# Optimization experiments

Hardware: AMD Instinct MI355X
Metric: run time of the kernel (lower is better)

## Reference

```python
import jax, jax.numpy as jnp
import numpy as np

HIDDEN_DIM = 2048
NUM_HEADS = 16
HEAD_DIM = HIDDEN_DIM // NUM_HEADS  # 128, used only as softmax temperature sqrt(HEAD_DIM)
RING_SIZE = 4
RANK = 0  # dist not initialized


def _hilbert_mapping(size: int) -> np.ndarray:
    """Boustrophedon (snake) scan over a ceil(sqrt(size)) grid; mapping[pos] = scan index."""
    grid = int(np.ceil(np.sqrt(size)))
    order = []
    for row in range(grid):
        cols = range(grid) if row % 2 == 0 else range(grid - 1, -1, -1)
        for col in cols:
            pos = row * grid + col
            if pos < size:
                order.append(pos)
    mapping = np.zeros(size, dtype=np.int64)
    mapping[np.asarray(order)] = np.arange(size, dtype=np.int64)
    return mapping


def setup_inputs() -> dict:
    key = jax.random.key(0)
    k1, k2 = jax.random.split(key)
    batch, seq_len = 2, 8192
    chunk = seq_len // RING_SIZE
    x = jax.random.normal(k1, (batch, seq_len, HIDDEN_DIM), dtype=jnp.float32)
    # the torch module draws fresh randn scores each ring iteration; lifted here for determinism
    scores = jax.random.normal(k2, (RING_SIZE, batch, chunk, chunk), dtype=jnp.float32)
    return {"x": x, "scores": scores}


def reference(x, scores):
    batch, seq_len, hidden = x.shape
    ring_size, _, chunk, _ = scores.shape
    mapping = jnp.asarray(_hilbert_mapping(seq_len))  # static wrt jit

    # Hilbert gather: x_hilbert[b, i] = x[b, mapping[i]]
    x_h = x[:, mapping, :]

    local_start = RANK * chunk
    local_chunk = jax.lax.dynamic_slice_in_dim(x_h, local_start, chunk, axis=1)  # [B, C, D]

    # softmax over last dim with temperature sqrt(head_dim), summed over ring iterations
    attn = jax.nn.softmax(scores / np.sqrt(HEAD_DIM).astype(np.float32), axis=-1)  # [R, B, C, C]
    acc = jnp.einsum('rbij,bjd->bid', attn, local_chunk)  # sum over ring iterations

    out = jnp.zeros_like(x_h)
    out = jax.lax.dynamic_update_slice_in_dim(out, acc, local_start, axis=1)

    # inverse Hilbert scatter via argsort(mapping)
    inv = jnp.argsort(mapping)
    return out[:, inv, :]
```

## Files before the change

### kernel.cpp

```cpp
#include <hip/hip_runtime.h>
#include <hip/hip_bf16.h>
#include <stdint.h>

#define RING 4
#define BATCH 2
#define SEQ 8192
#define CHUNK 2048
#define HIDDEN 2048
#define G91 91

typedef unsigned short u16;
typedef __bf16 bf16x8 __attribute__((ext_vector_type(8)));
typedef float f32x4 __attribute__((ext_vector_type(4)));

__device__ __forceinline__ int hmap(int p) {
    int row = p / G91;
    int col = p - row * G91;
    return row * G91 + ((row & 1) ? (G91 - 1 - col) : col);
}

__device__ __forceinline__ u16 f2bf(float f) {
    unsigned int u = __float_as_uint(f);
    u = u + 0x7fffu + ((u >> 16) & 1u);
    return (u16)(u >> 16);
}

__global__ __launch_bounds__(256) void zero_tail(float4* __restrict__ out4) {
    const int per_batch = (SEQ - CHUNK) * (HIDDEN / 4);
    int idx = blockIdx.x * 256 + threadIdx.x;
    int b = idx >= per_batch;
    int within = idx - b * per_batch;
    long base = ((long)b * SEQ + CHUNK) * (HIDDEN / 4);
    out4[base + within] = make_float4(0.f, 0.f, 0.f, 0.f);
}

__global__ __launch_bounds__(256) void softmax_sum(const float* __restrict__ scores,
                                                   u16* __restrict__ P) {
    const float scale = 0.08838834764831845f;
    int bi = blockIdx.x;
    int b = bi >> 11;
    int i = bi & (CHUNK - 1);
    int t = threadIdx.x;
    int w = t >> 6, lane = t & 63;

    float4 v[RING][2];
#pragma unroll
    for (int r = 0; r < RING; ++r) {
        const float4* src = (const float4*)scores +
            ((((long)(r * BATCH + b) * CHUNK + i) * CHUNK) >> 2);
        v[r][0] = src[t];
        v[r][1] = src[t + 256];
    }
    float* pv = (float*)v;
#pragma unroll
    for (int q = 0; q < RING * 8; ++q) pv[q] *= scale;

    float lm[RING];
#pragma unroll
    for (int r = 0; r < RING; ++r) {
        float* a = (float*)&v[r][0];
        float m0 = fmaxf(fmaxf(a[0], a[1]), fmaxf(a[2], a[3]));
        float m1 = fmaxf(fmaxf(a[4], a[5]), fmaxf(a[6], a[7]));
        lm[r] = fmaxf(m0, m1);
    }
#pragma unroll
    for (int off = 32; off >= 1; off >>= 1)
#pragma unroll
        for (int r = 0; r < RING; ++r)
            lm[r] = fmaxf(lm[r], __shfl_xor(lm[r], off, 64));
    __shared__ float red[4][RING];
    if (lane == 0) {
#pragma unroll
        for (int r = 0; r < RING; ++r) red[w][r] = lm[r];
    }
    __syncthreads();
    float m[RING];
#pragma unroll
    for (int r = 0; r < RING; ++r)
        m[r] = fmaxf(fmaxf(red[0][r], red[1][r]), fmaxf(red[2][r], red[3][r]));
    __syncthreads();

    float e[RING][8];
    float ls[RING];
#pragma unroll
    for (int r = 0; r < RING; ++r) {
        float* a = (float*)&v[r][0];
        ls[r] = 0.f;
#pragma unroll
        for (int q = 0; q < 8; ++q) {
            e[r][q] = __expf(a[q] - m[r]);
            ls[r] += e[r][q];
        }
    }
#pragma unroll
    for (int off = 32; off >= 1; off >>= 1)
#pragma unroll
        for (int r = 0; r < RING; ++r)
            ls[r] += __shfl_xor(ls[r], off, 64);
    if (lane == 0) {
#pragma unroll
        for (int r = 0; r < RING; ++r) red[w][r] = ls[r];
    }
    __syncthreads();
    float zi[RING];
#pragma unroll
    for (int r = 0; r < RING; ++r)
        zi[r] = 1.0f / (red[0][r] + red[1][r] + red[2][r] + red[3][r]);

    float p[8];
#pragma unroll
    for (int q = 0; q < 8; ++q)
        p[q] = e[0][q] * zi[0] + e[1][q] * zi[1] + e[2][q] * zi[2] + e[3][q] * zi[3];

    u16* dst = P + ((long)b * CHUNK + i) * CHUNK;
    *(uint2*)(dst + t * 4) = make_uint2(
        (unsigned)f2bf(p[0]) | ((unsigned)f2bf(p[1]) << 16),
        (unsigned)f2bf(p[2]) | ((unsigned)f2bf(p[3]) << 16));
    *(uint2*)(dst + 1024 + t * 4) = make_uint2(
        (unsigned)f2bf(p[4]) | ((unsigned)f2bf(p[5]) << 16),
        (unsigned)f2bf(p[6]) | ((unsigned)f2bf(p[7]) << 16));
}

__global__ __launch_bounds__(256) void gather_transpose(const float* __restrict__ x,
                                                        u16* __restrict__ xlT) {
    __shared__ u16 lt[64][72];
    int blk = blockIdx.x;
    int b = blk >> 10;
    int tile = blk & 1023;
    int j0 = (tile >> 5) << 6;
    int d0 = (tile & 31) << 6;
    int t = threadIdx.x;
    int jr = t >> 2;
    int dq = t & 3;
    int srow = hmap(j0 + jr);
    const float4* src = (const float4*)(x + ((long)b * SEQ + srow) * HIDDEN + d0) + dq * 4;
#pragma unroll
    for (int q = 0; q < 4; ++q) {
        float4 vv = src[q];
        int dd = dq * 16 + q * 4;
        lt[dd + 0][jr] = f2bf(vv.x);
        lt[dd + 1][jr] = f2bf(vv.y);
        lt[dd + 2][jr] = f2bf(vv.z);
        lt[dd + 3][jr] = f2bf(vv.w);
    }
    __syncthreads();
    int d = t >> 2;
    int jb = (t & 3) * 16;
    u16* dst = xlT + ((long)b * HIDDEN + d0 + d) * CHUNK + j0 + jb;
    uint4 w0 = *(const uint4*)&lt[d][jb];
    uint4 w1 = *(const uint4*)&lt[d][jb + 8];
    *(uint4*)dst = w0;
    *((uint4*)(dst + 8)) = w1;
}

__global__ __launch_bounds__(256) void gemm_scatter(const u16* __restrict__ P,
                                                    const u16* __restrict__ xlT,
                                                    float* __restrict__ out) {
    __shared__ u16 As[128 * 64];
    __shared__ u16 Bs[128 * 64];
    int blk = blockIdx.x;
    int b = blk >> 8;
    int tl = blk & 255;
    int ti = tl >> 4, tj = tl & 15;
    const int i0 = ti << 7, n0 = tj << 7;
    const u16* A = P + (long)b * CHUNK * CHUNK;
    const u16* B = xlT + (long)b * HIDDEN * CHUNK;
    int t = threadIdx.x, w = t >> 6, lane = t & 63;
    int wr = w >> 1, wc = w & 1;
    int srow = lane >> 3;
    int skb = (lane & 7) ^ srow;

    f32x4 z = {0.f, 0.f, 0.f, 0.f};
    f32x4 acc[4][4];
#pragma unroll
    for (int m = 0; m < 4; ++m)
#pragma unroll
        for (int n = 0; n < 4; ++n) acc[m][n] = z;

    for (int k0 = 0; k0 < CHUNK; k0 += 64) {
        __syncthreads();
#pragma unroll
        for (int seg = 0; seg < 4; ++seg) {
            int q = (w << 2) + seg;
            int grow = (q << 3) + srow;
            const u16* ga = A + (long)(i0 + grow) * CHUNK + k0 + (skb << 3);
            const u16* gb = B + (long)(n0 + grow) * CHUNK + k0 + (skb << 3);
            __builtin_amdgcn_global_load_lds(
                (const __attribute__((address_space(1))) void*)ga,
                (__attribute__((address_space(3))) void*)(As + (q << 9)), 16, 0, 0);
            __builtin_amdgcn_global_load_lds(
                (const __attribute__((address_space(1))) void*)gb,
                (__attribute__((address_space(3))) void*)(Bs + (q << 9)), 16, 0, 0);
        }
        __syncthreads();
#pragma unroll
        for (int ks = 0; ks < 2; ++ks) {
            int kb = (ks << 2) + (lane >> 4);
            bf16x8 fa[4], fb[4];
#pragma unroll
            for (int m = 0; m < 4; ++m) {
                int row = (wr << 6) + (m << 4) + (lane & 15);
                int phys = (row << 3) + (kb ^ (row & 7));
                fa[m] = *(const bf16x8*)(As + (phys << 3));
            }
#pragma unroll
            for (int n = 0; n < 4; ++n) {
                int row = (wc << 6) + (n << 4) + (lane & 15);
                int phys = (row << 3) + (kb ^ (row & 7));
                fb[n] = *(const bf16x8*)(Bs + (phys << 3));
            }
#pragma unroll
            for (int m = 0; m < 4; ++m)
#pragma unroll
                for (int n = 0; n < 4; ++n)
                    acc[m][n] = __builtin_amdgcn_mfma_f32_16x16x32_bf16(
                        fa[m], fb[n], acc[m][n], 0, 0, 0);
        }
    }

    int cr = (lane >> 4) << 2;
    int cc = lane & 15;
#pragma unroll
    for (int m = 0; m < 4; ++m) {
#pragma unroll
        for (int r = 0; r < 4; ++r) {
            int i = i0 + (wr << 6) + (m << 4) + cr + r;
            int orow = hmap(i);
            float* op = out + ((long)b * SEQ + orow) * HIDDEN + n0 + (wc << 6) + cc;
#pragma unroll
            for (int n = 0; n < 4; ++n) op[n << 4] = acc[m][n][r];
        }
    }
}

extern "C" void kernel_launch(void* const* d_in, const int* in_sizes, int n_in,
                              void* d_out, int out_size, void* d_ws, size_t ws_size,
                              hipStream_t stream) {
    const float* x = (const float*)d_in[0];
    const float* scores = (const float*)d_in[1];
    float* out = (float*)d_out;

    const size_t elems = (size_t)BATCH * CHUNK * CHUNK;
    u16 *Pp, *xlT;
    if (ws_size >= 2 * elems * sizeof(u16)) {
        Pp = (u16*)d_ws;
        xlT = (u16*)d_ws + elems;
    } else {
        Pp = (u16*)(out + (size_t)CHUNK * HIDDEN);
        xlT = (u16*)(out + (size_t)2 * CHUNK * HIDDEN);
    }

    softmax_sum<<<BATCH * CHUNK, 256, 0, stream>>>(scores, Pp);
    gather_transpose<<<2048, 256, 0, stream>>>(x, xlT);
    gemm_scatter<<<BATCH * 256, 256, 0, stream>>>(Pp, xlT, out);
    zero_tail<<<(BATCH * (SEQ - CHUNK) * (HIDDEN / 4)) / 256, 256, 0, stream>>>((float4*)out);
}
```

Measured before the change: 339.8 us.

## Double-buffer GEMM LDS tiles and fold tail zeroing into GEMM kernel

The GEMM kernel now keeps two LDS buffers, so the async global-to-LDS load of the next K tile is issued before the MFMAs on the current tile, with one barrier per iteration instead of two. When the workspace is large enough, each GEMM block also zeroes a slice of the output tail, which removes the separate zero_tail launch. LDS use per block doubles to 64 KB, which may reduce occupancy. The zeroing stores add write traffic at the start of every GEMM block.

```diff
diff --git a/kernel.cpp b/kernel.cpp
--- a/kernel.cpp
+++ b/kernel.cpp
@@ -155,9 +155,10 @@
 
 __global__ __launch_bounds__(256) void gemm_scatter(const u16* __restrict__ P,
                                                     const u16* __restrict__ xlT,
-                                                    float* __restrict__ out) {
-    __shared__ u16 As[128 * 64];
-    __shared__ u16 Bs[128 * 64];
+                                                    float* __restrict__ out,
+                                                    int zflag) {
+    __shared__ u16 As[2][128 * 64];
+    __shared__ u16 Bs[2][128 * 64];
     int blk = blockIdx.x;
     int b = blk >> 8;
     int tl = blk & 255;
@@ -170,6 +171,21 @@
     int srow = lane >> 3;
     int skb = (lane & 7) ^ srow;
 
+    if (zflag) {
+        const int span = (SEQ - CHUNK) * (HIDDEN / 4);
+        const long base0 = (long)CHUNK * (HIDDEN / 4);
+        const long base1 = (long)(SEQ + CHUNK) * (HIDDEN / 4);
+        float4* o4 = (float4*)out;
+        const float4 z4 = make_float4(0.f, 0.f, 0.f, 0.f);
+#pragma unroll
+        for (int q = 0; q < 48; ++q) {
+            int idx = blk * 12288 + q * 256 + t;
+            int bb = idx >= span;
+            int off = idx - (bb ? span : 0);
+            o4[(bb ? base1 : base0) + off] = z4;
+        }
+    }
+
     f32x4 z = {0.f, 0.f, 0.f, 0.f};
     f32x4 acc[4][4];
 #pragma unroll
@@ -177,8 +193,7 @@
 #pragma unroll
         for (int n = 0; n < 4; ++n) acc[m][n] = z;
 
-    for (int k0 = 0; k0 < CHUNK; k0 += 64) {
-        __syncthreads();
+    auto stage = [&](int pb, int k0) {
 #pragma unroll
         for (int seg = 0; seg < 4; ++seg) {
             int q = (w << 2) + seg;
@@ -187,12 +202,20 @@
             const u16* gb = B + (long)(n0 + grow) * CHUNK + k0 + (skb << 3);
             __builtin_amdgcn_global_load_lds(
                 (const __attribute__((address_space(1))) void*)ga,
-                (__attribute__((address_space(3))) void*)(As + (q << 9)), 16, 0, 0);
+                (__attribute__((address_space(3))) void*)(&As[pb][q << 9]), 16, 0, 0);
             __builtin_amdgcn_global_load_lds(
                 (const __attribute__((address_space(1))) void*)gb,
-                (__attribute__((address_space(3))) void*)(Bs + (q << 9)), 16, 0, 0);
-        }
-        __syncthreads();
+                (__attribute__((address_space(3))) void*)(&Bs[pb][q << 9]), 16, 0, 0);
+        }
+    };
+
+    stage(0, 0);
+    __syncthreads();
+
+    const int NT = CHUNK / 64;
+    for (int it = 0; it < NT; ++it) {
+        int cur = it & 1;
+        if (it + 1 < NT) stage(cur ^ 1, (it + 1) << 6);
 #pragma unroll
         for (int ks = 0; ks < 2; ++ks) {
             int kb = (ks << 2) + (lane >> 4);
@@ -201,13 +224,13 @@
             for (int m = 0; m < 4; ++m) {
                 int row = (wr << 6) + (m << 4) + (lane & 15);
                 int phys = (row << 3) + (kb ^ (row & 7));
-                fa[m] = *(const bf16x8*)(As + (phys << 3));
+                fa[m] = *(const bf16x8*)(&As[cur][phys << 3]);
             }
 #pragma unroll
             for (int n = 0; n < 4; ++n) {
                 int row = (wc << 6) + (n << 4) + (lane & 15);
                 int phys = (row << 3) + (kb ^ (row & 7));
-                fb[n] = *(const bf16x8*)(Bs + (phys << 3));
+                fb[n] = *(const bf16x8*)(&Bs[cur][phys << 3]);
             }
 #pragma unroll
             for (int m = 0; m < 4; ++m)
@@ -216,6 +239,7 @@
                     acc[m][n] = __builtin_amdgcn_mfma_f32_16x16x32_bf16(
                         fa[m], fb[n], acc[m][n], 0, 0, 0);
         }
+        __syncthreads();
     }
 
     int cr = (lane >> 4) << 2;
@@ -242,7 +266,8 @@
 
     const size_t elems = (size_t)BATCH * CHUNK * CHUNK;
     u16 *Pp, *xlT;
-    if (ws_size >= 2 * elems * sizeof(u16)) {
+    bool ws_ok = (ws_size >= 2 * elems * sizeof(u16));
+    if (ws_ok) {
         Pp = (u16*)d_ws;
         xlT = (u16*)d_ws + elems;
     } else {
@@ -252,6 +277,7 @@
 
     softmax_sum<<<BATCH * CHUNK, 256, 0, stream>>>(scores, Pp);
     gather_transpose<<<2048, 256, 0, stream>>>(x, xlT);
-    gemm_scatter<<<BATCH * 256, 256, 0, stream>>>(Pp, xlT, out);
-    zero_tail<<<(BATCH * (SEQ - CHUNK) * (HIDDEN / 4)) / 256, 256, 0, stream>>>((float4*)out);
-}
+    gemm_scatter<<<BATCH * 256, 256, 0, stream>>>(Pp, xlT, out, ws_ok ? 1 : 0);
+    if (!ws_ok)
+        zero_tail<<<(BATCH * (SEQ - CHUNK) * (HIDDEN / 4)) / 256, 256, 0, stream>>>((float4*)out);
+}
```

New measurement: 334.9 us. About the same (-1.4%).
